# Kernel tuning notes

Hardware: AMD Instinct MI355X
Metric: run time of the kernel (lower is better)

## Reference

```python
import jax, jax.numpy as jnp
import numpy as np

D_IN = 1024
D_OUT = 1024
SEQ = 4096


def setup_inputs() -> dict:
    key = jax.random.key(0)
    kx, kq, kk, kv = jax.random.split(key, 4)
    s = 1.0 / np.sqrt(D_IN)
    return {
        "x": jax.random.normal(kx, (SEQ, D_IN), dtype=jnp.float32),
        # nn.Linear weights: shape [d_out, d_in], applied as x @ W.T
        "W_q": jax.random.uniform(kq, (D_OUT, D_IN), dtype=jnp.float32, minval=-s, maxval=s),
        "W_k": jax.random.uniform(kk, (D_OUT, D_IN), dtype=jnp.float32, minval=-s, maxval=s),
        "W_v": jax.random.uniform(kv, (D_OUT, D_IN), dtype=jnp.float32, minval=-s, maxval=s),
    }


def reference(x, W_q, W_k, W_v):
    # QKV projections (no bias)
    q = x @ W_q.T  # [N, d_out]
    k = x @ W_k.T
    v = x @ W_v.T
    d_k = k.shape[-1]
    scores = (q @ k.T) / jnp.sqrt(jnp.asarray(d_k, x.dtype))  # [N, N]
    attn = jax.nn.softmax(scores, axis=1)
    n = attn.shape[0]
    mask = jnp.tril(jnp.ones((n, n), dtype=attn.dtype))
    causal = attn * mask
    causal = causal / jnp.sum(causal, axis=1, keepdims=True)
    return causal @ v  # [N, d_out]
```

## Files before the change

### kernel.cpp

```cpp
#include <hip/hip_runtime.h>
#include <hip/hip_bf16.h>
#include <stdint.h>
#include <math.h>

#define SEQ 4096
#define DIM 1024

typedef __attribute__((ext_vector_type(8))) __bf16 bf16x8;
typedef __attribute__((ext_vector_type(4))) float f32x4;
typedef __attribute__((ext_vector_type(8))) unsigned short u16x8;

__device__ __forceinline__ unsigned short f2bf(float f) {
  unsigned int u = __float_as_uint(f);
  u = (u + 0x7FFFu + ((u >> 16) & 1u)) >> 16;
  return (unsigned short)u;
}

__device__ __forceinline__ int swz(int o) { return o ^ (((o >> 7) & 7) << 4); }

template <int N> __device__ __forceinline__ void wait_vm() {
  if constexpr (N == 0) asm volatile("s_waitcnt vmcnt(0)" ::: "memory");
  else if constexpr (N == 4) asm volatile("s_waitcnt vmcnt(4)" ::: "memory");
  else if constexpr (N == 6) asm volatile("s_waitcnt vmcnt(6)" ::: "memory");
  else if constexpr (N == 8) asm volatile("s_waitcnt vmcnt(8)" ::: "memory");
}

__global__ void __launch_bounds__(256) cvt_all(const float* __restrict__ x,
                                               const float* __restrict__ wq,
                                               const float* __restrict__ wk,
                                               const float* __restrict__ wv,
                                               unsigned short* __restrict__ xb,
                                               unsigned short* __restrict__ wqk,
                                               unsigned short* __restrict__ wvb) {
  const int bid = blockIdx.x;
  const float* src;
  unsigned short* dst;
  size_t base;
  if (bid < 2048)      { src = x;  dst = xb;                base = (size_t)bid * 2048; }
  else if (bid < 2560) { src = wq; dst = wqk;               base = (size_t)(bid - 2048) * 2048; }
  else if (bid < 3072) { src = wk; dst = wqk + 1024 * 1024; base = (size_t)(bid - 2560) * 2048; }
  else                 { src = wv; dst = wvb;               base = (size_t)(bid - 3072) * 2048; }
  size_t i = base + (size_t)threadIdx.x * 8;
  float4 a = *reinterpret_cast<const float4*>(src + i);
  float4 b = *reinterpret_cast<const float4*>(src + i + 4);
  u16x8 o;
  o[0] = f2bf(a.x); o[1] = f2bf(a.y); o[2] = f2bf(a.z); o[3] = f2bf(a.w);
  o[4] = f2bf(b.x); o[5] = f2bf(b.y); o[6] = f2bf(b.z); o[7] = f2bf(b.w);
  *reinterpret_cast<u16x8*>(dst + i) = o;
}

__device__ __forceinline__ void gemm128s(const unsigned short* __restrict__ A,
                                         const unsigned short* __restrict__ B,
                                         unsigned short* __restrict__ C,
                                         unsigned short* As, unsigned short* Bs,
                                         int lda, int ldb, int ldc,
                                         int tr, int tc, float scale) {
  constexpr int NT = 32;
  const int tid = threadIdx.x;
  const int lane = tid & 63;
  const int wid = tid >> 6;
  const int wr = wid >> 1, wc = wid & 1;
  const int l15 = lane & 15;
  const int kq = lane >> 4;

  f32x4 acc[4][4];
  #pragma unroll
  for (int m = 0; m < 4; ++m)
    #pragma unroll
    for (int n = 0; n < 4; ++n)
      acc[m][n] = (f32x4){0.f, 0.f, 0.f, 0.f};

  const unsigned short* Abase = A + (size_t)tr * 128 * lda;
  const unsigned short* Bbase = B + (size_t)tc * 128 * ldb;

  auto stage = [&](int buf, int kt) {
    const int k0 = kt << 5;
    #pragma unroll
    for (int i = 0; i < 2; ++i) {
      const int idx = i * 256 + tid;
      const int row = idx >> 2;
      const int cs = (idx & 3) ^ (row & 3);
      const unsigned short* ga = Abase + (size_t)row * lda + k0 + cs * 8;
      const unsigned short* gb = Bbase + (size_t)row * ldb + k0 + cs * 8;
      __builtin_amdgcn_global_load_lds(
          (const __attribute__((address_space(1))) unsigned int*)ga,
          (__attribute__((address_space(3))) unsigned int*)(As + buf * 4096 + idx * 8), 16, 0, 0);
      __builtin_amdgcn_global_load_lds(
          (const __attribute__((address_space(1))) unsigned int*)gb,
          (__attribute__((address_space(3))) unsigned int*)(Bs + buf * 4096 + idx * 8), 16, 0, 0);
    }
  };

  stage(0, 0);
  int cur = 0;
  for (int kt = 0; kt < NT; ++kt) {
    if (kt + 1 < NT) { stage(cur ^ 1, kt + 1); wait_vm<4>(); }
    else wait_vm<0>();
    __builtin_amdgcn_s_barrier();

    bf16x8 af[4], bv[4];
    #pragma unroll
    for (int m = 0; m < 4; ++m) {
      const int row = wr * 64 + m * 16 + l15;
      const int o = (row << 6) + ((kq ^ (row & 3)) << 4);
      af[m] = *reinterpret_cast<const bf16x8*>((const char*)(As + cur * 4096) + o);
    }
    #pragma unroll
    for (int n = 0; n < 4; ++n) {
      const int row = wc * 64 + n * 16 + l15;
      const int o = (row << 6) + ((kq ^ (row & 3)) << 4);
      bv[n] = *reinterpret_cast<const bf16x8*>((const char*)(Bs + cur * 4096) + o);
    }
    __builtin_amdgcn_s_setprio(1);
    #pragma unroll
    for (int m = 0; m < 4; ++m)
      #pragma unroll
      for (int n = 0; n < 4; ++n)
        acc[m][n] = __builtin_amdgcn_mfma_f32_16x16x32_bf16(af[m], bv[n], acc[m][n], 0, 0, 0);
    __builtin_amdgcn_s_setprio(0);
    __builtin_amdgcn_s_barrier();
    cur ^= 1;
  }

  const int rbase = tr * 128 + wr * 64 + kq * 4;
  const int cbase = tc * 128 + wc * 64 + l15;
  #pragma unroll
  for (int m = 0; m < 4; ++m)
    #pragma unroll
    for (int n = 0; n < 4; ++n)
      #pragma unroll
      for (int i = 0; i < 4; ++i)
        C[(size_t)(rbase + m * 16 + i) * ldc + cbase + n * 16] = f2bf(acc[m][n][i] * scale);
}

__global__ void __launch_bounds__(256) projvt_kernel(const unsigned short* __restrict__ xb,
                                                     const unsigned short* __restrict__ wqk,
                                                     const unsigned short* __restrict__ wvb,
                                                     unsigned short* __restrict__ qkb,
                                                     unsigned short* __restrict__ vt) {
  __shared__ __align__(16) unsigned short As[2 * 128 * 32];
  __shared__ __align__(16) unsigned short Bs[2 * 128 * 32];
  const int bid = blockIdx.x;
  if (bid < 512) {
    gemm128s(xb, wqk, qkb, As, Bs, DIM, DIM, 2048, bid >> 4, bid & 15, 1.0f);
  } else {
    const int t = bid - 512;
    gemm128s(wvb, xb, vt, As, Bs, DIM, DIM, SEQ, t >> 5, t & 31, 1.0f);
  }
}

__global__ void __launch_bounds__(256) qkt_kernel(const unsigned short* __restrict__ qkb,
                                                  unsigned short* __restrict__ S) {
  __shared__ __align__(16) unsigned short As[2 * 128 * 32];
  __shared__ __align__(16) unsigned short Bs[2 * 128 * 32];
  const int b = blockIdx.x;
  int tr = (int)((sqrtf(8.0f * b + 1.0f) - 1.0f) * 0.5f);
  while ((tr + 1) * (tr + 2) / 2 <= b) ++tr;
  while (tr * (tr + 1) / 2 > b) --tr;
  const int tc = b - tr * (tr + 1) / 2;
  gemm128s(qkb, qkb + 1024, S, As, Bs, 2048, 2048, SEQ, tr, tc, 0.03125f);
}

__global__ void __launch_bounds__(256) pv_kernel(const unsigned short* __restrict__ A,
                                                 const unsigned short* __restrict__ B,
                                                 float* __restrict__ C,
                                                 float* __restrict__ P1, float* __restrict__ P2,
                                                 float* __restrict__ P3) {
  constexpr int BM = 64;
  constexpr int lda = SEQ, ldb = SEQ, ldc = DIM;
  int tc = blockIdx.x, tr = blockIdx.y;
  const int s = blockIdx.z;
  const int ltiles = tr + 1;
  int kt0 = s * 16;
  if (kt0 >= ltiles) return;
  const int nt = min(ltiles, kt0 + 16) - kt0;

  __shared__ __align__(16) unsigned short As[2][BM * 64];
  __shared__ __align__(16) unsigned short Bs[2][128 * 64];

  const int tid = threadIdx.x;
  const int lane = tid & 63;
  const int wid = tid >> 6;
  const int wr = wid >> 1, wc = wid & 1;
  const int l15 = lane & 15;
  const int kq = lane >> 4;

  f32x4 acc[2][4];
  #pragma unroll
  for (int m = 0; m < 2; ++m)
    #pragma unroll
    for (int n = 0; n < 4; ++n)
      acc[m][n] = (f32x4){0.f, 0.f, 0.f, 0.f};

  const unsigned short* Abase = A + (size_t)tr * BM * lda;
  const unsigned short* Bbase = B + (size_t)tc * 128 * ldb;

  auto stage = [&](int buf, int ktabs) {
    const int k0 = ktabs << 6;
    #pragma unroll
    for (int i = 0; i < 2; ++i) {
      const int o = (i * 256 + tid) * 16;
      const int cs = (swz(o) >> 4) & 7;
      const unsigned short* g = Abase + (size_t)(o >> 7) * lda + k0 + cs * 8;
      __builtin_amdgcn_global_load_lds(
          (const __attribute__((address_space(1))) unsigned int*)g,
          (__attribute__((address_space(3))) unsigned int*)((char*)&As[buf][0] + o), 16, 0, 0);
    }
    #pragma unroll
    for (int i = 0; i < 4; ++i) {
      const int o = (i * 256 + tid) * 16;
      const int cs = (swz(o) >> 4) & 7;
      const unsigned short* g = Bbase + (size_t)(o >> 7) * ldb + k0 + cs * 8;
      __builtin_amdgcn_global_load_lds(
          (const __attribute__((address_space(1))) unsigned int*)g,
          (__attribute__((address_space(3))) unsigned int*)((char*)&Bs[buf][0] + o), 16, 0, 0);
    }
  };

  stage(0, kt0);
  int cur = 0;
  for (int kt = 0; kt < nt; ++kt) {
    if (kt + 1 < nt) { stage(cur ^ 1, kt0 + kt + 1); wait_vm<6>(); }
    else wait_vm<0>();
    __builtin_amdgcn_s_barrier();

    bf16x8 af[2][2], bv[4][2];
    #pragma unroll
    for (int m = 0; m < 2; ++m)
      #pragma unroll
      for (int ks = 0; ks < 2; ++ks) {
        const int row = wr * 32 + m * 16 + l15;
        af[m][ks] = *reinterpret_cast<const bf16x8*>(
            (const char*)&As[cur][0] + swz(row * 128 + kq * 16 + ks * 64));
      }
    #pragma unroll
    for (int n = 0; n < 4; ++n)
      #pragma unroll
      for (int ks = 0; ks < 2; ++ks) {
        const int row = wc * 64 + n * 16 + l15;
        bv[n][ks] = *reinterpret_cast<const bf16x8*>(
            (const char*)&Bs[cur][0] + swz(row * 128 + kq * 16 + ks * 64));
      }
    #pragma unroll
    for (int m = 0; m < 2; ++m)
      #pragma unroll
      for (int n = 0; n < 4; ++n) {
        acc[m][n] = __builtin_amdgcn_mfma_f32_16x16x32_bf16(af[m][0], bv[n][0], acc[m][n], 0, 0, 0);
        acc[m][n] = __builtin_amdgcn_mfma_f32_16x16x32_bf16(af[m][1], bv[n][1], acc[m][n], 0, 0, 0);
      }
    __builtin_amdgcn_s_barrier();
    cur ^= 1;
  }

  float* fdst = C;
  int rowoff = 0;
  if (s == 1) { fdst = P1; rowoff = 1024; }
  else if (s == 2) { fdst = P2; rowoff = 2048; }
  else if (s == 3) { fdst = P3; rowoff = 3072; }
  const int rbase = tr * BM + wr * 32 + kq * 4;
  const int cbase = tc * 128 + wc * 64 + l15;
  #pragma unroll
  for (int m = 0; m < 2; ++m)
    #pragma unroll
    for (int n = 0; n < 4; ++n)
      #pragma unroll
      for (int i = 0; i < 4; ++i)
        fdst[(size_t)(rbase + m * 16 + i - rowoff) * ldc + cbase + n * 16] = acc[m][n][i];
}

__global__ void __launch_bounds__(256) reduce_kernel(float* __restrict__ out,
                                                     const float* __restrict__ p1,
                                                     const float* __restrict__ p2,
                                                     const float* __restrict__ p3) {
  const int b = blockIdx.x;
  const size_t e = ((size_t)b * 1024) + threadIdx.x * 4;
  f32x4 acc = *reinterpret_cast<f32x4*>(out + (size_t)1024 * 1024 + e);
  acc += *reinterpret_cast<const f32x4*>(p1 + e);
  if (b >= 1024) acc += *reinterpret_cast<const f32x4*>(p2 + e - (size_t)1024 * 1024);
  if (b >= 2048) acc += *reinterpret_cast<const f32x4*>(p3 + e - (size_t)2048 * 1024);
  *reinterpret_cast<f32x4*>(out + (size_t)1024 * 1024 + e) = acc;
}

__global__ void __launch_bounds__(256) softmax_causal(unsigned short* __restrict__ S) {
  const int row = blockIdx.x;
  const int limit = ((row >> 6) + 1) << 6;
  unsigned short* Srow = S + (size_t)row * SEQ;
  const int tid = threadIdx.x;
  const int lane = tid & 63, wid = tid >> 6;

  float vals[16];
  bool act[2];
  #pragma unroll
  for (int i = 0; i < 2; ++i) {
    const int j0 = (tid + i * 256) * 8;
    act[i] = j0 < limit;
    if (act[i]) {
      const uint4 w = *reinterpret_cast<const uint4*>(Srow + j0);
      const unsigned int wb[4] = {w.x, w.y, w.z, w.w};
      #pragma unroll
      for (int e = 0; e < 4; ++e) {
        vals[i * 8 + 2 * e]     = __uint_as_float(wb[e] << 16);
        vals[i * 8 + 2 * e + 1] = __uint_as_float(wb[e] & 0xFFFF0000u);
      }
    } else {
      #pragma unroll
      for (int e = 0; e < 8; ++e) vals[i * 8 + e] = -1e30f;
    }
  }

  float m = -1e30f;
  #pragma unroll
  for (int i = 0; i < 2; ++i)
    #pragma unroll
    for (int e = 0; e < 8; ++e) {
      int j = (tid + i * 256) * 8 + e;
      if (j <= row) m = fmaxf(m, vals[i * 8 + e]);
    }
  #pragma unroll
  for (int off = 32; off > 0; off >>= 1) m = fmaxf(m, __shfl_xor(m, off));
  __shared__ float redm[4], reds[4];
  if (lane == 0) redm[wid] = m;
  __syncthreads();
  m = fmaxf(fmaxf(redm[0], redm[1]), fmaxf(redm[2], redm[3]));

  float s = 0.f;
  float ev[16];
  #pragma unroll
  for (int i = 0; i < 2; ++i)
    #pragma unroll
    for (int e = 0; e < 8; ++e) {
      int j = (tid + i * 256) * 8 + e;
      float ex = (j <= row) ? __expf(vals[i * 8 + e] - m) : 0.f;
      ev[i * 8 + e] = ex;
      s += ex;
    }
  #pragma unroll
  for (int off = 32; off > 0; off >>= 1) s += __shfl_xor(s, off);
  if (lane == 0) reds[wid] = s;
  __syncthreads();
  s = reds[0] + reds[1] + reds[2] + reds[3];
  const float inv = 1.f / s;

  #pragma unroll
  for (int i = 0; i < 2; ++i) {
    if (!act[i]) continue;
    u16x8 o;
    #pragma unroll
    for (int e = 0; e < 8; ++e) o[e] = f2bf(ev[i * 8 + e] * inv);
    *reinterpret_cast<u16x8*>(Srow + (tid + i * 256) * 8) = o;
  }
}

extern "C" void kernel_launch(void* const* d_in, const int* in_sizes, int n_in,
                              void* d_out, int out_size, void* d_ws, size_t ws_size,
                              hipStream_t stream) {
  const float* x  = (const float*)d_in[0];
  const float* Wq = (const float*)d_in[1];
  const float* Wk = (const float*)d_in[2];
  const float* Wv = (const float*)d_in[3];
  float* out = (float*)d_out;

  char* ws = (char*)d_ws;
  const size_t MB = 1u << 20;
  unsigned short* xb   = (unsigned short*)(ws + 0 * MB);
  unsigned short* wqk  = (unsigned short*)(ws + 8 * MB);
  unsigned short* wvb  = (unsigned short*)(ws + 12 * MB);
  unsigned short* qkb  = (unsigned short*)(ws + 14 * MB);
  unsigned short* vt   = (unsigned short*)(ws + 30 * MB);
  unsigned short* S    = (unsigned short*)(ws + 38 * MB);
  float* p1 = (float*)(ws + 0 * MB);
  float* p2 = (float*)(ws + 12 * MB);
  float* p3 = (float*)(ws + 20 * MB);

  cvt_all<<<3584, 256, 0, stream>>>(x, Wq, Wk, Wv, xb, wqk, wvb);

  projvt_kernel<<<768, 256, 0, stream>>>(xb, wqk, wvb, qkb, vt);

  qkt_kernel<<<528, 256, 0, stream>>>(qkb, S);

  softmax_causal<<<SEQ, 256, 0, stream>>>(S);

  pv_kernel<<<dim3(DIM / 128, SEQ / 64, 4), 256, 0, stream>>>(S, vt, out, p1, p2, p3);
  reduce_kernel<<<3072, 256, 0, stream>>>(out, p1, p2, p3);
}
```

Before: 136.5 us.

## Double GEMM K-tile to 64 with XOR swizzle and XCD-aware block remap

The shared 128x128 bf16 GEMM helper now stages K-tiles of 64 instead of 32, which halves the number of barrier-separated iterations and doubles the MFMA work per sync. LDS addressing switches to an 8-way XOR swizzle over 128-byte rows to avoid bank conflicts. The projection and QK^T kernels also remap blockIdx so consecutive blocks across the 8 XCDs cover neighbouring tiles, aiming for better L2 locality. LDS use per block doubles to 64KB, which may reduce occupancy.

```diff
diff --git a/kernel.cpp b/kernel.cpp
--- a/kernel.cpp
+++ b/kernel.cpp
@@ -20,7 +20,6 @@
 
 template <int N> __device__ __forceinline__ void wait_vm() {
   if constexpr (N == 0) asm volatile("s_waitcnt vmcnt(0)" ::: "memory");
-  else if constexpr (N == 4) asm volatile("s_waitcnt vmcnt(4)" ::: "memory");
   else if constexpr (N == 6) asm volatile("s_waitcnt vmcnt(6)" ::: "memory");
   else if constexpr (N == 8) asm volatile("s_waitcnt vmcnt(8)" ::: "memory");
 }
@@ -49,13 +48,13 @@
   *reinterpret_cast<u16x8*>(dst + i) = o;
 }
 
-__device__ __forceinline__ void gemm128s(const unsigned short* __restrict__ A,
-                                         const unsigned short* __restrict__ B,
-                                         unsigned short* __restrict__ C,
-                                         unsigned short* As, unsigned short* Bs,
-                                         int lda, int ldb, int ldc,
-                                         int tr, int tc, float scale) {
-  constexpr int NT = 32;
+__device__ __forceinline__ void gemm128_64(const unsigned short* __restrict__ A,
+                                           const unsigned short* __restrict__ B,
+                                           unsigned short* __restrict__ C,
+                                           unsigned short* As, unsigned short* Bs,
+                                           int lda, int ldb, int ldc,
+                                           int tr, int tc, float scale) {
+  constexpr int NT = 16;
   const int tid = threadIdx.x;
   const int lane = tid & 63;
   const int wid = tid >> 6;
@@ -74,49 +73,54 @@
   const unsigned short* Bbase = B + (size_t)tc * 128 * ldb;
 
   auto stage = [&](int buf, int kt) {
-    const int k0 = kt << 5;
-    #pragma unroll
-    for (int i = 0; i < 2; ++i) {
-      const int idx = i * 256 + tid;
-      const int row = idx >> 2;
-      const int cs = (idx & 3) ^ (row & 3);
-      const unsigned short* ga = Abase + (size_t)row * lda + k0 + cs * 8;
-      const unsigned short* gb = Bbase + (size_t)row * ldb + k0 + cs * 8;
+    const int k0 = kt << 6;
+    #pragma unroll
+    for (int i = 0; i < 4; ++i) {
+      const int o = (i * 256 + tid) * 16;
+      const int cs = (swz(o) >> 4) & 7;
+      const unsigned short* ga = Abase + (size_t)(o >> 7) * lda + k0 + cs * 8;
+      const unsigned short* gb = Bbase + (size_t)(o >> 7) * ldb + k0 + cs * 8;
       __builtin_amdgcn_global_load_lds(
           (const __attribute__((address_space(1))) unsigned int*)ga,
-          (__attribute__((address_space(3))) unsigned int*)(As + buf * 4096 + idx * 8), 16, 0, 0);
+          (__attribute__((address_space(3))) unsigned int*)((char*)(As + buf * 8192) + o), 16, 0, 0);
       __builtin_amdgcn_global_load_lds(
           (const __attribute__((address_space(1))) unsigned int*)gb,
-          (__attribute__((address_space(3))) unsigned int*)(Bs + buf * 4096 + idx * 8), 16, 0, 0);
+          (__attribute__((address_space(3))) unsigned int*)((char*)(Bs + buf * 8192) + o), 16, 0, 0);
     }
   };
 
   stage(0, 0);
   int cur = 0;
   for (int kt = 0; kt < NT; ++kt) {
-    if (kt + 1 < NT) { stage(cur ^ 1, kt + 1); wait_vm<4>(); }
+    if (kt + 1 < NT) { stage(cur ^ 1, kt + 1); wait_vm<8>(); }
     else wait_vm<0>();
     __builtin_amdgcn_s_barrier();
 
-    bf16x8 af[4], bv[4];
-    #pragma unroll
-    for (int m = 0; m < 4; ++m) {
-      const int row = wr * 64 + m * 16 + l15;
-      const int o = (row << 6) + ((kq ^ (row & 3)) << 4);
-      af[m] = *reinterpret_cast<const bf16x8*>((const char*)(As + cur * 4096) + o);
-    }
-    #pragma unroll
-    for (int n = 0; n < 4; ++n) {
-      const int row = wc * 64 + n * 16 + l15;
-      const int o = (row << 6) + ((kq ^ (row & 3)) << 4);
-      bv[n] = *reinterpret_cast<const bf16x8*>((const char*)(Bs + cur * 4096) + o);
-    }
+    bf16x8 af[4][2], bv[4][2];
+    #pragma unroll
+    for (int m = 0; m < 4; ++m)
+      #pragma unroll
+      for (int ks = 0; ks < 2; ++ks) {
+        const int row = wr * 64 + m * 16 + l15;
+        af[m][ks] = *reinterpret_cast<const bf16x8*>(
+            (const char*)(As + cur * 8192) + swz(row * 128 + kq * 16 + ks * 64));
+      }
+    #pragma unroll
+    for (int n = 0; n < 4; ++n)
+      #pragma unroll
+      for (int ks = 0; ks < 2; ++ks) {
+        const int row = wc * 64 + n * 16 + l15;
+        bv[n][ks] = *reinterpret_cast<const bf16x8*>(
+            (const char*)(Bs + cur * 8192) + swz(row * 128 + kq * 16 + ks * 64));
+      }
     __builtin_amdgcn_s_setprio(1);
     #pragma unroll
     for (int m = 0; m < 4; ++m)
       #pragma unroll
-      for (int n = 0; n < 4; ++n)
-        acc[m][n] = __builtin_amdgcn_mfma_f32_16x16x32_bf16(af[m], bv[n], acc[m][n], 0, 0, 0);
+      for (int n = 0; n < 4; ++n) {
+        acc[m][n] = __builtin_amdgcn_mfma_f32_16x16x32_bf16(af[m][0], bv[n][0], acc[m][n], 0, 0, 0);
+        acc[m][n] = __builtin_amdgcn_mfma_f32_16x16x32_bf16(af[m][1], bv[n][1], acc[m][n], 0, 0, 0);
+      }
     __builtin_amdgcn_s_setprio(0);
     __builtin_amdgcn_s_barrier();
     cur ^= 1;
@@ -138,27 +142,27 @@
                                                      const unsigned short* __restrict__ wvb,
                                                      unsigned short* __restrict__ qkb,
                                                      unsigned short* __restrict__ vt) {
-  __shared__ __align__(16) unsigned short As[2 * 128 * 32];
-  __shared__ __align__(16) unsigned short Bs[2 * 128 * 32];
-  const int bid = blockIdx.x;
+  __shared__ __align__(16) unsigned short As[2 * 128 * 64];
+  __shared__ __align__(16) unsigned short Bs[2 * 128 * 64];
+  const int bid = (blockIdx.x & 7) * 96 + (blockIdx.x >> 3);
   if (bid < 512) {
-    gemm128s(xb, wqk, qkb, As, Bs, DIM, DIM, 2048, bid >> 4, bid & 15, 1.0f);
+    gemm128_64(xb, wqk, qkb, As, Bs, DIM, DIM, 2048, bid >> 4, bid & 15, 1.0f);
   } else {
     const int t = bid - 512;
-    gemm128s(wvb, xb, vt, As, Bs, DIM, DIM, SEQ, t >> 5, t & 31, 1.0f);
+    gemm128_64(wvb, xb, vt, As, Bs, DIM, DIM, SEQ, t >> 5, t & 31, 1.0f);
   }
 }
 
 __global__ void __launch_bounds__(256) qkt_kernel(const unsigned short* __restrict__ qkb,
                                                   unsigned short* __restrict__ S) {
-  __shared__ __align__(16) unsigned short As[2 * 128 * 32];
-  __shared__ __align__(16) unsigned short Bs[2 * 128 * 32];
-  const int b = blockIdx.x;
+  __shared__ __align__(16) unsigned short As[2 * 128 * 64];
+  __shared__ __align__(16) unsigned short Bs[2 * 128 * 64];
+  const int b = (blockIdx.x & 7) * 66 + (blockIdx.x >> 3);
   int tr = (int)((sqrtf(8.0f * b + 1.0f) - 1.0f) * 0.5f);
   while ((tr + 1) * (tr + 2) / 2 <= b) ++tr;
   while (tr * (tr + 1) / 2 > b) --tr;
   const int tc = b - tr * (tr + 1) / 2;
-  gemm128s(qkb, qkb + 1024, S, As, Bs, 2048, 2048, SEQ, tr, tc, 0.03125f);
+  gemm128_64(qkb, qkb + 1024, S, As, Bs, 2048, 2048, SEQ, tr, tc, 0.03125f);
 }
 
 __global__ void __launch_bounds__(256) pv_kernel(const unsigned short* __restrict__ A,
```

Result: slower. 141.3 us (+3.5%).
